# Kernel tuning notes

Measured on AMD Instinct MI355X. Metric: run time of the kernel, lower is better.

The kernel has to match this reference:

```python
import jax, jax.numpy as jnp
import numpy as np

B, T, D, VQ, L2, HID = 8, 2048, 768, 64, 12, 1024
K = 2 ** L2          # 4096 codebook entries
N_MID = 4            # condition_layer=6 -> 1 input + 4 middle + 1 output Linear, 5 BatchNorms
EPS_N = 1e-6
EPS_BN = 1e-5


def setup_inputs() -> dict:
    key = jax.random.key(0)
    ks = jax.random.split(key, 10)
    g = lambda i, shape, sc: jax.random.normal(ks[i], shape, jnp.float32) * sc
    return {
        "h_in": jax.random.normal(ks[0], (B, D, T), jnp.float32),
        "attn_mask": jax.random.randint(ks[1], (B, T), 0, 2, jnp.int32),
        "proj_w": g(2, (VQ, D), 0.02), "proj_b": jnp.zeros((VQ,), jnp.float32),
        "inv_w": g(3, (D, VQ), 0.02), "inv_b": jnp.zeros((D,), jnp.float32),
        "mlp_w_in": g(4, (HID, L2), 0.1), "mlp_b_in": jnp.zeros((HID,), jnp.float32),
        "mlp_w_mid": g(5, (N_MID, HID, HID), 0.03), "mlp_b_mid": jnp.zeros((N_MID, HID), jnp.float32),
        "mlp_w_out": g(6, (VQ, HID), 0.03), "mlp_b_out": jnp.zeros((VQ,), jnp.float32),
        "bn_gamma": jnp.ones((N_MID + 1, HID), jnp.float32),
        "bn_beta": jnp.zeros((N_MID + 1, HID), jnp.float32),
    }


def _bn(x, gamma, beta):
    # BatchNorm1d, training mode: batch mean / biased var over codebook rows
    m = x.mean(axis=0)
    v = x.var(axis=0)
    return (x - m) * jax.lax.rsqrt(v + EPS_BN) * gamma + beta


def _l2norm(x):
    return x / (jnp.linalg.norm(x, axis=-1, keepdims=True) + EPS_N)


def reference(h_in, attn_mask, proj_w, proj_b, inv_w, inv_b,
              mlp_w_in, mlp_b_in, mlp_w_mid, mlp_b_mid, mlp_w_out, mlp_b_out,
              bn_gamma, bn_beta):
    # --- codebook: binary vectors -> condition MLP (Linear+BN+ReLU x5, Linear) ---
    ints = jnp.arange(K)
    bits = ((ints[:, None] & (1 << jnp.arange(L2 - 1, -1, -1))) > 0).astype(jnp.float32)  # [K, L2]
    x = jax.nn.relu(_bn(bits @ mlp_w_in.T + mlp_b_in, bn_gamma[0], bn_beta[0]))
    for i in range(N_MID):
        x = jax.nn.relu(_bn(x @ mlp_w_mid[i].T + mlp_b_mid[i], bn_gamma[i + 1], bn_beta[i + 1]))
    embed = x @ mlp_w_out.T + mlp_b_out          # [K, VQ]
    embed = _l2norm(embed)                        # sphere=True

    # --- project hidden states: h_in [B,D,T] -> [B,T,VQ] ---
    h = jnp.einsum('bdt,vd->btv', h_in, proj_w) + proj_b
    h = _l2norm(h)

    # --- pairwise squared distances to codebook, argmax of -d (== softmax argmax) ---
    hf = h.reshape(-1, VQ)                                       # [B*T, VQ]
    d = (hf ** 2).sum(-1, keepdims=True) + (embed ** 2).sum(-1) - 2.0 * (hf @ embed.T)  # [B*T, K]
    code = jnp.argmax(-d, axis=-1)                               # [B*T]

    # --- masked gather/scatter quantization (eval path: hard codes) ---
    mask = (attn_mask == 1)                                      # [B, T]
    h_vq = embed[code].reshape(B, T, VQ) * mask[..., None].astype(h.dtype)
    quantized = jnp.einsum('btv,dv->btd', h_vq, inv_w) + inv_b   # proj_inv -> [B, T, D]
    vq_code = jnp.where(mask, code.reshape(B, T), 0)
    return quantized, vq_code
```

## Files before the change

### kernel.cpp

```cpp
#include <hip/hip_runtime.h>
#include <stddef.h>

#define BB   8
#define TT_  2048
#define DD   768
#define VQ_  64
#define L2C  12
#define HID_ 1024
#define KK   4096
#define NMID 4
#define NT   (BB*TT_)

typedef _Float16 h8v __attribute__((ext_vector_type(8)));
typedef float    f4v __attribute__((ext_vector_type(4)));

#define LDA 40

__global__ __launch_bounds__(256) void k_mlp_in(const float* __restrict__ w_in,
                                                const float* __restrict__ b_in,
                                                float* __restrict__ X) {
    __shared__ float ws_[256 * 12];
    __shared__ float bs_[256];
    int tid = threadIdx.x;
    int h0  = blockIdx.x * 256;
    for (int i = tid; i < 256 * 12; i += 256) ws_[i] = w_in[h0 * 12 + i];
    bs_[tid] = b_in[h0 + tid];
    __syncthreads();
    float w[12];
#pragma unroll
    for (int l = 0; l < 12; l++) w[l] = ws_[tid * 12 + l];
    float bias = bs_[tid];
    int k0 = blockIdx.y * 16;
    for (int kk = 0; kk < 16; kk++) {
        int k = k0 + kk;
        float acc = bias;
#pragma unroll
        for (int l = 0; l < 12; l++)
            if ((k >> (11 - l)) & 1) acc += w[l];
        X[(size_t)k * HID_ + h0 + tid] = acc;
    }
}

__global__ __launch_bounds__(256) void k_bn_stats1(const float* __restrict__ Y,
                                                   float* __restrict__ part) {
    int b = blockIdx.x;
    int c = blockIdx.y * 256 + threadIdx.x;
    const float* src = Y + ((size_t)b << 6) * HID_ + c;
    float s = 0.f, q = 0.f;
    for (int r = 0; r < 64; r++) {
        float v = src[(size_t)r << 10];
        s += v; q += v * v;
    }
    part[((size_t)b << 10) + c] = s;
    part[65536 + ((size_t)b << 10) + c] = q;
}

__global__ __launch_bounds__(256) void k_bn_stats2(const float* __restrict__ part,
                                                   float* __restrict__ mv) {
    int c = blockIdx.x * 256 + threadIdx.x;
    float s = 0.f, q = 0.f;
    for (int b = 0; b < 64; b++) {
        s += part[((size_t)b << 10) + c];
        q += part[65536 + ((size_t)b << 10) + c];
    }
    float m = s * (1.f / KK);
    float v = q * (1.f / KK) - m * m;
    mv[c] = m; mv[HID_ + c] = v;
}

__global__ __launch_bounds__(256) void k_bn_apply_split(const float* __restrict__ Y,
                                                        const float* __restrict__ mv,
                                                        const float* __restrict__ gamma,
                                                        const float* __restrict__ beta,
                                                        _Float16* __restrict__ Xhi,
                                                        _Float16* __restrict__ Xlo) {
    int i = blockIdx.x * 256 + threadIdx.x;
    int c = (i << 2) & (HID_ - 1);
    float4 x = ((const float4*)Y)[i];
    float4 m = *(const float4*)(mv + c);
    float4 v = *(const float4*)(mv + HID_ + c);
    float4 g = *(const float4*)(gamma + c);
    float4 b = *(const float4*)(beta + c);
    float o[4];
    o[0] = fmaxf(0.f, (x.x - m.x) * (1.f / sqrtf(v.x + 1e-5f)) * g.x + b.x);
    o[1] = fmaxf(0.f, (x.y - m.y) * (1.f / sqrtf(v.y + 1e-5f)) * g.y + b.y);
    o[2] = fmaxf(0.f, (x.z - m.z) * (1.f / sqrtf(v.z + 1e-5f)) * g.z + b.z);
    o[3] = fmaxf(0.f, (x.w - m.w) * (1.f / sqrtf(v.w + 1e-5f)) * g.w + b.w);
    union { _Float16 h[4]; uint2 u; } uh, ul;
#pragma unroll
    for (int j = 0; j < 4; j++) {
        _Float16 h = (_Float16)o[j];
        uh.h[j] = h;
        ul.h[j] = (_Float16)(o[j] - (float)h);
    }
    *(uint2*)(Xhi + ((size_t)i << 2)) = uh.u;
    *(uint2*)(Xlo + ((size_t)i << 2)) = ul.u;
}

__global__ __launch_bounds__(256) void k_gemm_mfma(const _Float16* __restrict__ Ahi,
                                                   const _Float16* __restrict__ Alo,
                                                   const float* __restrict__ W,
                                                   const float* __restrict__ bias,
                                                   float* __restrict__ C,
                                                   int M, int N, int Kd) {
    __shared__ _Float16 sAh[128 * LDA];
    __shared__ _Float16 sAl[128 * LDA];
    __shared__ _Float16 sWh[64 * LDA];
    __shared__ _Float16 sWl[64 * LDA];
    const int tid = threadIdx.x;
    const int m0 = blockIdx.x * 128, n0 = blockIdx.y * 64;
    const int wave = tid >> 6, lane = tid & 63;
    const int wm = (wave >> 1) << 6;
    const int wn = (wave & 1) << 5;
    const int l15 = lane & 15, quad = lane >> 4;

    const int ar = tid >> 1;
    const int ak = (tid & 1) << 4;
    const int wr = tid >> 2;
    const int wk = (tid & 3) << 3;

    f4v acc[4][2];
#pragma unroll
    for (int i = 0; i < 4; i++)
#pragma unroll
        for (int j = 0; j < 2; j++) acc[i][j] = (f4v){0.f, 0.f, 0.f, 0.f};

    const size_t abase = (size_t)(m0 + ar) * Kd + ak;
    const size_t wbase = (size_t)(n0 + wr) * Kd + wk;

    for (int k0 = 0; k0 < Kd; k0 += 32) {
        uint4 a0 = *(const uint4*)(Ahi + abase + k0);
        uint4 a1 = *(const uint4*)(Ahi + abase + k0 + 8);
        uint4 c0 = *(const uint4*)(Alo + abase + k0);
        uint4 c1 = *(const uint4*)(Alo + abase + k0 + 8);
        float4 w0 = *(const float4*)(W + wbase + k0);
        float4 w1 = *(const float4*)(W + wbase + k0 + 4);
        union { _Float16 h[8]; uint4 u; } wh, wl;
        float wf[8] = {w0.x, w0.y, w0.z, w0.w, w1.x, w1.y, w1.z, w1.w};
#pragma unroll
        for (int j = 0; j < 8; j++) {
            _Float16 h = (_Float16)wf[j];
            wh.h[j] = h;
            wl.h[j] = (_Float16)(wf[j] - (float)h);
        }
        __syncthreads();
        *(uint4*)(sAh + ar * LDA + ak)     = a0;
        *(uint4*)(sAh + ar * LDA + ak + 8) = a1;
        *(uint4*)(sAl + ar * LDA + ak)     = c0;
        *(uint4*)(sAl + ar * LDA + ak + 8) = c1;
        *(uint4*)(sWh + wr * LDA + wk) = wh.u;
        *(uint4*)(sWl + wr * LDA + wk) = wl.u;
        __syncthreads();

        h8v ah[4], alv[4], bh[2], bl[2];
#pragma unroll
        for (int i = 0; i < 4; i++) {
            ah[i]  = *(const h8v*)(sAh + (wm + (i << 4) + l15) * LDA + (quad << 3));
            alv[i] = *(const h8v*)(sAl + (wm + (i << 4) + l15) * LDA + (quad << 3));
        }
#pragma unroll
        for (int j = 0; j < 2; j++) {
            bh[j] = *(const h8v*)(sWh + (wn + (j << 4) + l15) * LDA + (quad << 3));
            bl[j] = *(const h8v*)(sWl + (wn + (j << 4) + l15) * LDA + (quad << 3));
        }
#pragma unroll
        for (int i = 0; i < 4; i++)
#pragma unroll
            for (int j = 0; j < 2; j++) {
                acc[i][j] = __builtin_amdgcn_mfma_f32_16x16x32_f16(ah[i],  bh[j], acc[i][j], 0, 0, 0);
                acc[i][j] = __builtin_amdgcn_mfma_f32_16x16x32_f16(ah[i],  bl[j], acc[i][j], 0, 0, 0);
                acc[i][j] = __builtin_amdgcn_mfma_f32_16x16x32_f16(alv[i], bh[j], acc[i][j], 0, 0, 0);
            }
    }
#pragma unroll
    for (int j = 0; j < 2; j++) {
        int col = n0 + wn + (j << 4) + l15;
        float bv = bias[col];
#pragma unroll
        for (int i = 0; i < 4; i++) {
            int row = m0 + wm + (i << 4) + (quad << 2);
#pragma unroll
            for (int r = 0; r < 4; r++)
                C[(size_t)(row + r) * N + col] = acc[i][j][r] + bv;
        }
    }
}

__global__ __launch_bounds__(256) void k_l2norm(float* __restrict__ E,
                                                float* __restrict__ eqh,
                                                _Float16* __restrict__ Ehi,
                                                _Float16* __restrict__ Elo) {
    int tid = threadIdx.x;
    int row = blockIdx.x * 4 + (tid >> 6);
    int v = tid & 63;
    size_t off = ((size_t)row << 6) + v;
    float x = E[off];
    float ss = x * x;
#pragma unroll
    for (int o = 32; o; o >>= 1) ss += __shfl_xor(ss, o, 64);
    float inv = 1.f / (sqrtf(ss) + 1e-6f);
    float xn = x * inv;
    E[off] = xn;
    _Float16 hh = (_Float16)xn;
    Ehi[off] = hh;
    Elo[off] = (_Float16)(xn - (float)hh);
    if (v == 0) eqh[row] = -0.5f * (ss * inv * inv);
}

__global__ __launch_bounds__(256) void k_wsplit(const float* __restrict__ pw,
                                                _Float16* __restrict__ pwhi,
                                                _Float16* __restrict__ pwlo) {
    int i = blockIdx.x * 256 + threadIdx.x;
    float4 w = ((const float4*)pw)[i];
    float wf[4] = {w.x, w.y, w.z, w.w};
    union { _Float16 h[4]; uint2 u; } uh, ul;
#pragma unroll
    for (int j = 0; j < 4; j++) {
        _Float16 h = (_Float16)wf[j];
        uh.h[j] = h;
        ul.h[j] = (_Float16)(wf[j] - (float)h);
    }
    *(uint2*)(pwhi + ((size_t)i << 2)) = uh.u;
    *(uint2*)(pwlo + ((size_t)i << 2)) = ul.u;
}

__global__ __launch_bounds__(256) void k_cvt_inv(const float* __restrict__ iw,
                                                 _Float16* __restrict__ iwh) {
    int i = blockIdx.x * 256 + threadIdx.x;
    float4 w = ((const float4*)iw)[i];
    union { _Float16 h[4]; uint2 u; } uh;
    uh.h[0] = (_Float16)w.x; uh.h[1] = (_Float16)w.y;
    uh.h[2] = (_Float16)w.z; uh.h[3] = (_Float16)w.w;
    *(uint2*)(iwh + ((size_t)i << 2)) = uh.u;
}

__global__ __launch_bounds__(256) void k_proj_mfma(const float* __restrict__ h_in,
                                                   const _Float16* __restrict__ pwhi,
                                                   const _Float16* __restrict__ pwlo,
                                                   float* __restrict__ Hpart) {
    __shared__ float shA[128 * 33];
    const int tid = threadIdx.x;
    const int t0 = blockIdx.x * 128;
    const int ks = blockIdx.y;
    const int b = t0 >> 11;
    const int tloc0 = t0 & (TT_ - 1);
    const int wave = tid >> 6, lane = tid & 63;
    const int l15 = lane & 15, quad = lane >> 4;

    const int dl = tid >> 3;
    const int tg = (tid & 7) << 4;

    f4v acc[2][4];
#pragma unroll
    for (int i = 0; i < 2; i++)
#pragma unroll
        for (int j = 0; j < 4; j++) acc[i][j] = (f4v){0.f, 0.f, 0.f, 0.f};

    for (int kk = 0; kk < 6; kk++) {
        int dd0 = ks * 192 + kk * 32;
        const float* src = h_in + ((size_t)(b * DD + dd0 + dl) << 11) + tloc0 + tg;
        float4 g0 = *(const float4*)(src);
        float4 g1 = *(const float4*)(src + 4);
        float4 g2 = *(const float4*)(src + 8);
        float4 g3 = *(const float4*)(src + 12);
        __syncthreads();
        float gv[16] = {g0.x, g0.y, g0.z, g0.w, g1.x, g1.y, g1.z, g1.w,
                        g2.x, g2.y, g2.z, g2.w, g3.x, g3.y, g3.z, g3.w};
#pragma unroll
        for (int i = 0; i < 16; i++) shA[(tg + i) * 33 + dl] = gv[i];
        __syncthreads();

        h8v ah[2], al[2];
#pragma unroll
        for (int mt = 0; mt < 2; mt++) {
            const float* ap = &shA[((wave << 5) + (mt << 4) + l15) * 33 + (quad << 3)];
            float4 a0 = *(const float4*)(ap);
            float4 a1 = *(const float4*)(ap + 4);
            float av[8] = {a0.x, a0.y, a0.z, a0.w, a1.x, a1.y, a1.z, a1.w};
#pragma unroll
            for (int j = 0; j < 8; j++) {
                _Float16 h = (_Float16)av[j];
                ah[mt][j] = h;
                al[mt][j] = (_Float16)(av[j] - (float)h);
            }
        }
#pragma unroll
        for (int nt = 0; nt < 4; nt++) {
            size_t wb = (size_t)((nt << 4) + l15) * DD + dd0 + (quad << 3);
            h8v bh = *(const h8v*)(pwhi + wb);
            h8v bl = *(const h8v*)(pwlo + wb);
#pragma unroll
            for (int mt = 0; mt < 2; mt++) {
                acc[mt][nt] = __builtin_amdgcn_mfma_f32_16x16x32_f16(ah[mt], bh, acc[mt][nt], 0, 0, 0);
                acc[mt][nt] = __builtin_amdgcn_mfma_f32_16x16x32_f16(ah[mt], bl, acc[mt][nt], 0, 0, 0);
                acc[mt][nt] = __builtin_amdgcn_mfma_f32_16x16x32_f16(al[mt], bh, acc[mt][nt], 0, 0, 0);
            }
        }
    }
    float* dst = Hpart + ((size_t)ks << 20);
#pragma unroll
    for (int mt = 0; mt < 2; mt++) {
#pragma unroll
        for (int r = 0; r < 4; r++) {
            int t = t0 + (wave << 5) + (mt << 4) + (quad << 2) + r;
#pragma unroll
            for (int nt = 0; nt < 4; nt++)
                dst[((size_t)t << 6) + (nt << 4) + l15] = acc[mt][nt][r];
        }
    }
}

__global__ __launch_bounds__(256) void k_hnorm(const float* __restrict__ Hpart,
                                               const float* __restrict__ pb,
                                               _Float16* __restrict__ Hhi,
                                               _Float16* __restrict__ Hlo) {
    __shared__ float ssp[4][64];
    int tid = threadIdx.x;
    int tt = tid & 63, vg = tid >> 6;
    int t = blockIdx.x * 64 + tt;
    size_t base = ((size_t)t << 6) + (vg << 4);
    float o[16];
#pragma unroll
    for (int u = 0; u < 4; u++) {
        float4 p0 = *(const float4*)(Hpart + (0u << 20) + base + (u << 2));
        float4 p1 = *(const float4*)(Hpart + (1u << 20) + base + (u << 2));
        float4 p2 = *(const float4*)(Hpart + (2u << 20) + base + (u << 2));
        float4 p3 = *(const float4*)(Hpart + (3u << 20) + base + (u << 2));
        o[u * 4 + 0] = p0.x + p1.x + p2.x + p3.x;
        o[u * 4 + 1] = p0.y + p1.y + p2.y + p3.y;
        o[u * 4 + 2] = p0.z + p1.z + p2.z + p3.z;
        o[u * 4 + 3] = p0.w + p1.w + p2.w + p3.w;
    }
    float sp = 0.f;
#pragma unroll
    for (int j = 0; j < 16; j++) {
        o[j] += pb[(vg << 4) + j];
        sp = fmaf(o[j], o[j], sp);
    }
    ssp[vg][tt] = sp;
    __syncthreads();
    float ss = ssp[0][tt] + ssp[1][tt] + ssp[2][tt] + ssp[3][tt];
    float inv = 1.f / (sqrtf(ss) + 1e-6f);
    union { _Float16 h[8]; uint4 u; } uh0, uh1, ul0, ul1;
#pragma unroll
    for (int j = 0; j < 16; j++) {
        float xn = o[j] * inv;
        _Float16 hh = (_Float16)xn;
        _Float16 ll = (_Float16)(xn - (float)hh);
        if (j < 8) { uh0.h[j] = hh; ul0.h[j] = ll; }
        else       { uh1.h[j - 8] = hh; ul1.h[j - 8] = ll; }
    }
    *(uint4*)(Hhi + base)     = uh0.u;
    *(uint4*)(Hhi + base + 8) = uh1.u;
    *(uint4*)(Hlo + base)     = ul0.u;
    *(uint4*)(Hlo + base + 8) = ul1.u;
}

__global__ __launch_bounds__(256) void k_argmax_mfma(const _Float16* __restrict__ Hhi,
                                                     const _Float16* __restrict__ Hlo,
                                                     const _Float16* __restrict__ Ehi,
                                                     const _Float16* __restrict__ Elo,
                                                     const float* __restrict__ eqh,
                                                     float* __restrict__ ps,
                                                     int* __restrict__ pi) {
    int tid = threadIdx.x;
    int wave = tid >> 6, lane = tid & 63;
    int l15 = lane & 15, quad = lane >> 4;
    int t0 = blockIdx.x * 256 + wave * 64;
    int kh = blockIdx.y;
    const int kbase = kh << 8;

    h8v hh0[4], hh1[4], hl0[4], hl1[4];
#pragma unroll
    for (int s = 0; s < 4; s++) {
        size_t hb = (size_t)(t0 + (s << 4) + l15) * 64 + (quad << 3);
        hh0[s] = *(const h8v*)(Hhi + hb);
        hh1[s] = *(const h8v*)(Hhi + hb + 32);
        hl0[s] = *(const h8v*)(Hlo + hb);
        hl1[s] = *(const h8v*)(Hlo + hb + 32);
    }
    float best[4] = {-1e30f, -1e30f, -1e30f, -1e30f};
    int   idx[4]  = {0, 0, 0, 0};

    size_t eb = (size_t)(kbase + l15) * 64 + (quad << 3);
    h8v eh0 = *(const h8v*)(Ehi + eb);
    h8v eh1 = *(const h8v*)(Ehi + eb + 32);
    h8v el0 = *(const h8v*)(Elo + eb);
    h8v el1 = *(const h8v*)(Elo + eb + 32);
    float4 q4 = *(const float4*)(eqh + kbase + (quad << 2));

    for (int it = 0; it < 16; it++) {
        h8v ce0 = eh0, ce1 = eh1, cl0 = el0, cl1 = el1;
        float4 cq = q4;
        int k0 = kbase + (it << 4);
        int kn = k0 + 16;
        if (kn > KK - 16) kn = KK - 16;
        size_t ebn = (size_t)(kn + l15) * 64 + (quad << 3);
        eh0 = *(const h8v*)(Ehi + ebn);
        eh1 = *(const h8v*)(Ehi + ebn + 32);
        el0 = *(const h8v*)(Elo + ebn);
        el1 = *(const h8v*)(Elo + ebn + 32);
        q4 = *(const float4*)(eqh + kn + (quad << 2));

        f4v acc[4];
#pragma unroll
        for (int s = 0; s < 4; s++) acc[s] = (f4v){0.f, 0.f, 0.f, 0.f};
#pragma unroll
        for (int s = 0; s < 4; s++) acc[s] = __builtin_amdgcn_mfma_f32_16x16x32_f16(ce0, hh0[s], acc[s], 0, 0, 0);
#pragma unroll
        for (int s = 0; s < 4; s++) acc[s] = __builtin_amdgcn_mfma_f32_16x16x32_f16(ce1, hh1[s], acc[s], 0, 0, 0);
#pragma unroll
        for (int s = 0; s < 4; s++) acc[s] = __builtin_amdgcn_mfma_f32_16x16x32_f16(cl0, hh0[s], acc[s], 0, 0, 0);
#pragma unroll
        for (int s = 0; s < 4; s++) acc[s] = __builtin_amdgcn_mfma_f32_16x16x32_f16(cl1, hh1[s], acc[s], 0, 0, 0);
#pragma unroll
        for (int s = 0; s < 4; s++) acc[s] = __builtin_amdgcn_mfma_f32_16x16x32_f16(ce0, hl0[s], acc[s], 0, 0, 0);
#pragma unroll
        for (int s = 0; s < 4; s++) acc[s] = __builtin_amdgcn_mfma_f32_16x16x32_f16(ce1, hl1[s], acc[s], 0, 0, 0);
        float qv[4] = {cq.x, cq.y, cq.z, cq.w};
#pragma unroll
        for (int r = 0; r < 4; r++) {
            int k = k0 + (quad << 2) + r;
#pragma unroll
            for (int s = 0; s < 4; s++) {
                float sc = acc[s][r] + qv[r];
                if (sc > best[s]) { best[s] = sc; idx[s] = k; }
            }
        }
    }
#pragma unroll
    for (int m = 16; m <= 32; m <<= 1) {
#pragma unroll
        for (int s = 0; s < 4; s++) {
            float ob = __shfl_xor(best[s], m, 64);
            int   oi = __shfl_xor(idx[s], m, 64);
            if (ob > best[s] || (ob == best[s] && oi < idx[s])) { best[s] = ob; idx[s] = oi; }
        }
    }
    if (quad == 0) {
#pragma unroll
        for (int s = 0; s < 4; s++) {
            int t = t0 + (s << 4) + l15;
            ps[(size_t)t * 16 + kh] = best[s];
            pi[(size_t)t * 16 + kh] = idx[s];
        }
    }
}

__global__ __launch_bounds__(256) void k_merge(const float* __restrict__ ps,
                                               const int* __restrict__ pi,
                                               const int* __restrict__ mask,
                                               const _Float16* __restrict__ Ehi,
                                               _Float16* __restrict__ G16,
                                               float* __restrict__ outc) {
    __shared__ int codes[256];
    __shared__ int ms[256];
    int tid = threadIdx.x;
    int base = blockIdx.x << 8;
    int t = base + tid;
    float best = ps[(size_t)t * 16];
    int bi = pi[(size_t)t * 16];
#pragma unroll
    for (int s = 1; s < 16; s++) {
        float v = ps[(size_t)t * 16 + s];
        if (v > best) { best = v; bi = pi[(size_t)t * 16 + s]; }
    }
    int m = mask[t];
    codes[tid] = bi;
    ms[tid] = m;
    outc[t] = m ? (float)bi : 0.0f;
    __syncthreads();
    for (int i = tid; i < 256 * 8; i += 256) {
        int r = i >> 3, u = i & 7;
        uint4 e = ms[r] ? ((const uint4*)(Ehi + ((size_t)codes[r] << 6)))[u]
                        : make_uint4(0u, 0u, 0u, 0u);
        ((uint4*)(G16 + ((size_t)(base + r) << 6)))[u] = e;
    }
}

__global__ __launch_bounds__(256) void k_gemm_out(const _Float16* __restrict__ G16,
                                                  const _Float16* __restrict__ iwh,
                                                  const float* __restrict__ bias,
                                                  float* __restrict__ C) {
    const int tid = threadIdx.x;
    const int t0 = blockIdx.x * 128, n0 = blockIdx.y * 64;
    const int wave = tid >> 6, lane = tid & 63;
    const int l15 = lane & 15, quad = lane >> 4;

    f4v acc[2][4];
#pragma unroll
    for (int i = 0; i < 2; i++)
#pragma unroll
        for (int j = 0; j < 4; j++) acc[i][j] = (f4v){0.f, 0.f, 0.f, 0.f};

#pragma unroll
    for (int ks = 0; ks < 2; ks++) {
        int kk = (ks << 5) + (quad << 3);
        h8v a[2], b[4];
#pragma unroll
        for (int mt = 0; mt < 2; mt++)
            a[mt] = *(const h8v*)(G16 + (size_t)(t0 + (wave << 5) + (mt << 4) + l15) * 64 + kk);
#pragma unroll
        for (int nt = 0; nt < 4; nt++)
            b[nt] = *(const h8v*)(iwh + (size_t)(n0 + (nt << 4) + l15) * 64 + kk);
#pragma unroll
        for (int mt = 0; mt < 2; mt++)
#pragma unroll
            for (int nt = 0; nt < 4; nt++)
                acc[mt][nt] = __builtin_amdgcn_mfma_f32_16x16x32_f16(a[mt], b[nt], acc[mt][nt], 0, 0, 0);
    }
#pragma unroll
    for (int nt = 0; nt < 4; nt++) {
        int col = n0 + (nt << 4) + l15;
        float bv = bias[col];
#pragma unroll
        for (int mt = 0; mt < 2; mt++) {
            int row = t0 + (wave << 5) + (mt << 4) + (quad << 2);
#pragma unroll
            for (int r = 0; r < 4; r++)
                C[(size_t)(row + r) * DD + col] = acc[mt][nt][r] + bv;
        }
    }
}

extern "C" void kernel_launch(void* const* d_in, const int* in_sizes, int n_in,
                              void* d_out, int out_size, void* d_ws, size_t ws_size,
                              hipStream_t stream) {
    const float* h_in   = (const float*)d_in[0];
    const int*   amask  = (const int*)d_in[1];
    const float* proj_w = (const float*)d_in[2];
    const float* proj_b = (const float*)d_in[3];
    const float* inv_w  = (const float*)d_in[4];
    const float* inv_b  = (const float*)d_in[5];
    const float* w_in   = (const float*)d_in[6];
    const float* b_in   = (const float*)d_in[7];
    const float* w_mid  = (const float*)d_in[8];
    const float* b_mid  = (const float*)d_in[9];
    const float* w_out  = (const float*)d_in[10];
    const float* b_out  = (const float*)d_in[11];
    const float* gamma  = (const float*)d_in[12];
    const float* beta   = (const float*)d_in[13];

    float*     Y    = (float*)d_ws;
    _Float16*  Xhi  = (_Float16*)(Y + (size_t)KK * HID_);
    _Float16*  Xlo  = Xhi + (size_t)KK * HID_;
    float*     mv   = (float*)(Xlo + (size_t)KK * HID_);
    float*     Emb  = mv + 2 * HID_;
    float*     eqh  = Emb + (size_t)KK * VQ_;
    float*     spart= eqh + KK;
    _Float16*  pwhi = (_Float16*)(spart + 2 * 65536);
    _Float16*  pwlo = pwhi + (size_t)VQ_ * DD;
    float*    Hpart = Y;
    _Float16* H16hi = Xhi;
    _Float16* H16lo = H16hi + (size_t)NT * VQ_;
    _Float16* E16hi = H16lo + (size_t)NT * VQ_;
    _Float16* E16lo = E16hi + (size_t)KK * VQ_;
    float*    ps    = (float*)(E16lo + (size_t)KK * VQ_);
    int*      pidx  = (int*)(ps + (size_t)NT * 16);
    _Float16* G16   = (_Float16*)(pidx + (size_t)NT * 16);
    _Float16* iwh   = G16 + (size_t)NT * VQ_;

    float* out_q = (float*)d_out;
    float* out_c = out_q + (size_t)NT * DD;

    k_mlp_in<<<dim3(HID_ / 256, KK / 16), 256, 0, stream>>>(w_in, b_in, Y);
    k_bn_stats1<<<dim3(64, 4), 256, 0, stream>>>(Y, spart);
    k_bn_stats2<<<4, 256, 0, stream>>>(spart, mv);
    k_bn_apply_split<<<KK * HID_ / 1024, 256, 0, stream>>>(Y, mv, gamma, beta, Xhi, Xlo);
    for (int i = 0; i < NMID; i++) {
        k_gemm_mfma<<<dim3(KK / 128, HID_ / 64), 256, 0, stream>>>(
            Xhi, Xlo, w_mid + (size_t)i * HID_ * HID_, b_mid + (size_t)i * HID_, Y,
            KK, HID_, HID_);
        k_bn_stats1<<<dim3(64, 4), 256, 0, stream>>>(Y, spart);
        k_bn_stats2<<<4, 256, 0, stream>>>(spart, mv);
        k_bn_apply_split<<<KK * HID_ / 1024, 256, 0, stream>>>(Y, mv,
            gamma + (size_t)(i + 1) * HID_, beta + (size_t)(i + 1) * HID_, Xhi, Xlo);
    }
    k_gemm_mfma<<<dim3(KK / 128, VQ_ / 64), 256, 0, stream>>>(
        Xhi, Xlo, w_out, b_out, Emb, KK, VQ_, HID_);
    k_l2norm<<<KK / 4, 256, 0, stream>>>(Emb, eqh, E16hi, E16lo);

    k_wsplit<<<VQ_ * DD / 1024, 256, 0, stream>>>(proj_w, pwhi, pwlo);
    k_cvt_inv<<<VQ_ * DD / 1024, 256, 0, stream>>>(inv_w, iwh);
    k_proj_mfma<<<dim3(NT / 128, 4), 256, 0, stream>>>(h_in, pwhi, pwlo, Hpart);
    k_hnorm<<<NT / 64, 256, 0, stream>>>(Hpart, proj_b, H16hi, H16lo);
    k_argmax_mfma<<<dim3(NT / 256, 16), 256, 0, stream>>>(
        H16hi, H16lo, E16hi, E16lo, eqh, ps, pidx);
    k_merge<<<NT / 256, 256, 0, stream>>>(ps, pidx, amask, E16hi, G16, out_c);
    k_gemm_out<<<dim3(NT / 128, DD / 64), 256, 0, stream>>>(G16, iwh, inv_b, out_q);
}
```

Before: 498.8 us.

## Rewrite MLP GEMM with async global-to-LDS double buffering and pre-split weights

The MLP GEMM kernel now takes weights that a separate k_wsplit launch has already split into fp16 hi/lo parts, so the per-tile float-to-half conversion leaves the inner loop. Tiles are staged through global_load_lds into double-buffered, XOR-swizzled LDS, so loading the next K-tile overlaps the MFMAs on the current one. The kernel also remaps workgroup indices and raises wave priority around the MFMA block. In exchange it adds extra wsplit launches and uses the output buffer as scratch for the split weights, which is only safe because the output is written later.

```diff
diff --git a/kernel.cpp b/kernel.cpp
--- a/kernel.cpp
+++ b/kernel.cpp
@@ -14,7 +14,9 @@
 typedef _Float16 h8v __attribute__((ext_vector_type(8)));
 typedef float    f4v __attribute__((ext_vector_type(4)));
 
-#define LDA 40
+#define GL16(g, l) __builtin_amdgcn_global_load_lds( \
+    (const __attribute__((address_space(1))) void*)(g), \
+    (__attribute__((address_space(3))) void*)(l), 16, 0, 0)
 
 __global__ __launch_bounds__(256) void k_mlp_in(const float* __restrict__ w_in,
                                                 const float* __restrict__ b_in,
@@ -97,27 +99,54 @@
     *(uint2*)(Xlo + ((size_t)i << 2)) = ul.u;
 }
 
-__global__ __launch_bounds__(256) void k_gemm_mfma(const _Float16* __restrict__ Ahi,
-                                                   const _Float16* __restrict__ Alo,
-                                                   const float* __restrict__ W,
-                                                   const float* __restrict__ bias,
-                                                   float* __restrict__ C,
-                                                   int M, int N, int Kd) {
-    __shared__ _Float16 sAh[128 * LDA];
-    __shared__ _Float16 sAl[128 * LDA];
-    __shared__ _Float16 sWh[64 * LDA];
-    __shared__ _Float16 sWl[64 * LDA];
+__global__ __launch_bounds__(256) void k_gemm_mfma2(const _Float16* __restrict__ Ahi,
+                                                    const _Float16* __restrict__ Alo,
+                                                    const _Float16* __restrict__ Whi,
+                                                    const _Float16* __restrict__ Wlo,
+                                                    const float* __restrict__ bias,
+                                                    float* __restrict__ C,
+                                                    int M, int N, int Kd) {
+    __shared__ __attribute__((aligned(128))) char lds[2][24576];
     const int tid = threadIdx.x;
-    const int m0 = blockIdx.x * 128, n0 = blockIdx.y * 64;
+    int wg = blockIdx.x;
+    const int nwg = gridDim.x;
+    wg = (wg & 7) * (nwg >> 3) + (wg >> 3);
+    const int nx = M >> 7;
+    const int m0 = (wg % nx) << 7;
+    const int n0 = (wg / nx) << 6;
     const int wave = tid >> 6, lane = tid & 63;
+    const int l15 = lane & 15, quad = lane >> 4;
     const int wm = (wave >> 1) << 6;
     const int wn = (wave & 1) << 5;
-    const int l15 = lane & 15, quad = lane >> 4;
-
-    const int ar = tid >> 1;
-    const int ak = (tid & 1) << 4;
-    const int wr = tid >> 2;
-    const int wk = (tid & 3) << 3;
+
+    const int pA0 = ((wave << 1) | 0) * 1024 + lane * 16;
+    const int pA1 = ((wave << 1) | 1) * 1024 + lane * 16;
+    const int pW  = wave * 1024 + lane * 16;
+    const int qA0 = pA0 ^ (((pA0 >> 7) & 3) << 4);
+    const int qA1 = pA1 ^ (((pA1 >> 7) & 3) << 4);
+    const int qW  = pW  ^ (((pW  >> 7) & 3) << 4);
+    const size_t krow = (size_t)Kd * 2;
+    const char* gAh0 = (const char*)Ahi + (size_t)(m0 + (qA0 >> 6)) * krow + (qA0 & 63);
+    const char* gAh1 = (const char*)Ahi + (size_t)(m0 + (qA1 >> 6)) * krow + (qA1 & 63);
+    const char* gAl0 = (const char*)Alo + (size_t)(m0 + (qA0 >> 6)) * krow + (qA0 & 63);
+    const char* gAl1 = (const char*)Alo + (size_t)(m0 + (qA1 >> 6)) * krow + (qA1 & 63);
+    const char* gWh  = (const char*)Whi + (size_t)(n0 + (qW >> 6)) * krow + (qW & 63);
+    const char* gWl  = (const char*)Wlo + (size_t)(n0 + (qW >> 6)) * krow + (qW & 63);
+    const int dA0 = (wave << 1) * 1024;
+    const int dA1 = dA0 + 1024;
+    const int dW  = wave * 1024;
+
+    int offA[4], offW[2];
+#pragma unroll
+    for (int i = 0; i < 4; i++) {
+        int r = wm + (i << 4) + l15;
+        offA[i] = r * 64 + ((quad ^ ((r >> 1) & 3)) << 4);
+    }
+#pragma unroll
+    for (int j = 0; j < 2; j++) {
+        int r = wn + (j << 4) + l15;
+        offW[j] = r * 64 + ((quad ^ ((r >> 1) & 3)) << 4);
+    }
 
     f4v acc[4][2];
 #pragma unroll
@@ -125,53 +154,55 @@
 #pragma unroll
         for (int j = 0; j < 2; j++) acc[i][j] = (f4v){0.f, 0.f, 0.f, 0.f};
 
-    const size_t abase = (size_t)(m0 + ar) * Kd + ak;
-    const size_t wbase = (size_t)(n0 + wr) * Kd + wk;
-
-    for (int k0 = 0; k0 < Kd; k0 += 32) {
-        uint4 a0 = *(const uint4*)(Ahi + abase + k0);
-        uint4 a1 = *(const uint4*)(Ahi + abase + k0 + 8);
-        uint4 c0 = *(const uint4*)(Alo + abase + k0);
-        uint4 c1 = *(const uint4*)(Alo + abase + k0 + 8);
-        float4 w0 = *(const float4*)(W + wbase + k0);
-        float4 w1 = *(const float4*)(W + wbase + k0 + 4);
-        union { _Float16 h[8]; uint4 u; } wh, wl;
-        float wf[8] = {w0.x, w0.y, w0.z, w0.w, w1.x, w1.y, w1.z, w1.w};
-#pragma unroll
-        for (int j = 0; j < 8; j++) {
-            _Float16 h = (_Float16)wf[j];
-            wh.h[j] = h;
-            wl.h[j] = (_Float16)(wf[j] - (float)h);
-        }
-        __syncthreads();
-        *(uint4*)(sAh + ar * LDA + ak)     = a0;
-        *(uint4*)(sAh + ar * LDA + ak + 8) = a1;
-        *(uint4*)(sAl + ar * LDA + ak)     = c0;
-        *(uint4*)(sAl + ar * LDA + ak + 8) = c1;
-        *(uint4*)(sWh + wr * LDA + wk) = wh.u;
-        *(uint4*)(sWl + wr * LDA + wk) = wl.u;
-        __syncthreads();
-
-        h8v ah[4], alv[4], bh[2], bl[2];
+#define STAGE(bufi, tt) do { \
+        char* b_ = lds[bufi]; size_t o_ = (size_t)(tt) << 6; \
+        GL16(gAh0 + o_, b_ + dA0); \
+        GL16(gAh1 + o_, b_ + dA1); \
+        GL16(gAl0 + o_, b_ + 8192 + dA0); \
+        GL16(gAl1 + o_, b_ + 8192 + dA1); \
+        GL16(gWh  + o_, b_ + 16384 + dW); \
+        GL16(gWl  + o_, b_ + 20480 + dW); \
+    } while (0)
+
+    STAGE(0, 0);
+    const int nt = Kd >> 5;
+    for (int t = 0; t < nt; ++t) {
+        const int cur = t & 1;
+        if (t + 1 < nt) {
+            STAGE(cur ^ 1, t + 1);
+            asm volatile("s_waitcnt vmcnt(6)" ::: "memory");
+        } else {
+            asm volatile("s_waitcnt vmcnt(0)" ::: "memory");
+        }
+        __builtin_amdgcn_s_barrier();
+        asm volatile("" ::: "memory");
+        const char* b = lds[cur];
+        h8v ah[4], al[4], bh[2], bl[2];
 #pragma unroll
         for (int i = 0; i < 4; i++) {
-            ah[i]  = *(const h8v*)(sAh + (wm + (i << 4) + l15) * LDA + (quad << 3));
-            alv[i] = *(const h8v*)(sAl + (wm + (i << 4) + l15) * LDA + (quad << 3));
+            ah[i] = *(const h8v*)(b + offA[i]);
+            al[i] = *(const h8v*)(b + 8192 + offA[i]);
         }
 #pragma unroll
         for (int j = 0; j < 2; j++) {
-            bh[j] = *(const h8v*)(sWh + (wn + (j << 4) + l15) * LDA + (quad << 3));
-            bl[j] = *(const h8v*)(sWl + (wn + (j << 4) + l15) * LDA + (quad << 3));
-        }
+            bh[j] = *(const h8v*)(b + 16384 + offW[j]);
+            bl[j] = *(const h8v*)(b + 20480 + offW[j]);
+        }
+        __builtin_amdgcn_s_setprio(1);
 #pragma unroll
         for (int i = 0; i < 4; i++)
 #pragma unroll
             for (int j = 0; j < 2; j++) {
-                acc[i][j] = __builtin_amdgcn_mfma_f32_16x16x32_f16(ah[i],  bh[j], acc[i][j], 0, 0, 0);
-                acc[i][j] = __builtin_amdgcn_mfma_f32_16x16x32_f16(ah[i],  bl[j], acc[i][j], 0, 0, 0);
-                acc[i][j] = __builtin_amdgcn_mfma_f32_16x16x32_f16(alv[i], bh[j], acc[i][j], 0, 0, 0);
+                acc[i][j] = __builtin_amdgcn_mfma_f32_16x16x32_f16(ah[i], bh[j], acc[i][j], 0, 0, 0);
+                acc[i][j] = __builtin_amdgcn_mfma_f32_16x16x32_f16(ah[i], bl[j], acc[i][j], 0, 0, 0);
+                acc[i][j] = __builtin_amdgcn_mfma_f32_16x16x32_f16(al[i], bh[j], acc[i][j], 0, 0, 0);
             }
-    }
+        __builtin_amdgcn_s_setprio(0);
+        asm volatile("" ::: "memory");
+        __builtin_amdgcn_s_barrier();
+    }
+#undef STAGE
+
 #pragma unroll
     for (int j = 0; j < 2; j++) {
         int col = n0 + wn + (j << 4) + l15;
@@ -563,21 +594,28 @@
     float* out_q = (float*)d_out;
     float* out_c = out_q + (size_t)NT * DD;
 
+    _Float16* Wmh = (_Float16*)d_out;
+    _Float16* Wml = Wmh + (size_t)HID_ * HID_;
+    _Float16* Woh = Wml + (size_t)HID_ * HID_;
+    _Float16* Wol = Woh + (size_t)VQ_ * HID_;
+
     k_mlp_in<<<dim3(HID_ / 256, KK / 16), 256, 0, stream>>>(w_in, b_in, Y);
     k_bn_stats1<<<dim3(64, 4), 256, 0, stream>>>(Y, spart);
     k_bn_stats2<<<4, 256, 0, stream>>>(spart, mv);
     k_bn_apply_split<<<KK * HID_ / 1024, 256, 0, stream>>>(Y, mv, gamma, beta, Xhi, Xlo);
     for (int i = 0; i < NMID; i++) {
-        k_gemm_mfma<<<dim3(KK / 128, HID_ / 64), 256, 0, stream>>>(
-            Xhi, Xlo, w_mid + (size_t)i * HID_ * HID_, b_mid + (size_t)i * HID_, Y,
-            KK, HID_, HID_);
+        k_wsplit<<<HID_ * HID_ / 1024, 256, 0, stream>>>(
+            w_mid + (size_t)i * HID_ * HID_, Wmh, Wml);
+        k_gemm_mfma2<<<(KK / 128) * (HID_ / 64), 256, 0, stream>>>(
+            Xhi, Xlo, Wmh, Wml, b_mid + (size_t)i * HID_, Y, KK, HID_, HID_);
         k_bn_stats1<<<dim3(64, 4), 256, 0, stream>>>(Y, spart);
         k_bn_stats2<<<4, 256, 0, stream>>>(spart, mv);
         k_bn_apply_split<<<KK * HID_ / 1024, 256, 0, stream>>>(Y, mv,
             gamma + (size_t)(i + 1) * HID_, beta + (size_t)(i + 1) * HID_, Xhi, Xlo);
     }
-    k_gemm_mfma<<<dim3(KK / 128, VQ_ / 64), 256, 0, stream>>>(
-        Xhi, Xlo, w_out, b_out, Emb, KK, VQ_, HID_);
+    k_wsplit<<<VQ_ * HID_ / 1024, 256, 0, stream>>>(w_out, Woh, Wol);
+    k_gemm_mfma2<<<(KK / 128) * (VQ_ / 64), 256, 0, stream>>>(
+        Xhi, Xlo, Woh, Wol, b_out, Emb, KK, VQ_, HID_);
     k_l2norm<<<KK / 4, 256, 0, stream>>>(Emb, eqh, E16hi, E16lo);
 
     k_wsplit<<<VQ_ * DD / 1024, 256, 0, stream>>>(proj_w, pwhi, pwlo);
```

Measured after the change: 518.3 us. 3.9% more time.
